# Kernel tuning notes

Hardware: AMD Instinct MI355X
Metric: run time of the kernel (lower is better)

Reference implementation:

```python
import jax, jax.numpy as jnp
import numpy as np

N = 50000      # nodes
E = 400000     # edges per relation
R = 3          # edge types
D = 128        # input_dim == hidden_dim
H = 8          # attention heads
Dh = D // H    # per-head dim (16)
OUT = 1        # output logits
NEG_SLOPE = 0.2
LN_EPS = 1e-5


def setup_inputs() -> dict:
    key = jax.random.key(0)
    ks = jax.random.split(key, 20)
    s = 0.05
    f32 = jnp.float32
    return {
        "feat": jax.random.normal(ks[0], (N, D), f32),
        "edge_src": jax.random.randint(ks[1], (R, E), 0, N, dtype=jnp.int32),
        "edge_dst": jax.random.randint(ks[2], (R, E), 0, N, dtype=jnp.int32),
        # conv1: per-relation GATConv params (W, attn_l, attn_r, bias)
        "W1": jax.random.normal(ks[3], (R, D, H * Dh), f32) * s,
        "al1": jax.random.normal(ks[4], (R, H, Dh), f32) * s,
        "ar1": jax.random.normal(ks[5], (R, H, Dh), f32) * s,
        "b1": jnp.zeros((R, H * Dh), f32),
        # conv2
        "W2": jax.random.normal(ks[6], (R, D, H * Dh), f32) * s,
        "al2": jax.random.normal(ks[7], (R, H, Dh), f32) * s,
        "ar2": jax.random.normal(ks[8], (R, H, Dh), f32) * s,
        "b2": jnp.zeros((R, H * Dh), f32),
        # LayerNorm
        "ln_g": jnp.ones((D,), f32),
        "ln_b": jnp.zeros((D,), f32),
        # classifier MLP (dropout inactive at eval)
        "Wc1": jax.random.normal(ks[9], (D, D), f32) * s,
        "bc1": jnp.zeros((D,), f32),
        "Wc2": jax.random.normal(ks[10], (D, OUT), f32) * s,
        "bc2": jnp.zeros((OUT,), f32),
    }


def _gat(x, src, dst, W, al, ar, b):
    """DGL GATConv on one relation: x [N,Din] -> [N, H*Dh]."""
    h = (x @ W).reshape(N, H, Dh)                       # projected feats
    el = (h * al).sum(-1)                               # [N,H] src attn term
    er = (h * ar).sum(-1)                               # [N,H] dst attn term
    e = jax.nn.leaky_relu(el[src] + er[dst], NEG_SLOPE)  # [E,H]
    # edge-softmax over incoming edges per dst node, per head
    m = jax.ops.segment_max(e, dst, num_segments=N)     # [N,H]
    ex = jnp.exp(e - m[dst])
    denom = jax.ops.segment_sum(ex, dst, num_segments=N)
    alpha = ex / denom[dst]                             # [E,H]
    msg = alpha[:, :, None] * h[src]                    # [E,H,Dh]
    out = jax.ops.segment_sum(msg, dst, num_segments=N)  # [N,H,Dh]
    return out.reshape(N, H * Dh) + b


def _hetero(x, edge_src, edge_dst, W, al, ar, b):
    out = jnp.zeros((N, H * Dh), x.dtype)
    for r in range(R):  # small fixed relation count
        out = out + _gat(x, edge_src[r], edge_dst[r], W[r], al[r], ar[r], b[r])
    return out


def reference(feat, edge_src, edge_dst, W1, al1, ar1, b1, W2, al2, ar2, b2,
              ln_g, ln_b, Wc1, bc1, Wc2, bc2):
    h1 = jax.nn.relu(_hetero(feat, edge_src, edge_dst, W1, al1, ar1, b1))
    h2 = _hetero(h1, edge_src, edge_dst, W2, al2, ar2, b2)
    h = h2 + h1
    mu = h.mean(-1, keepdims=True)
    var = ((h - mu) ** 2).mean(-1, keepdims=True)
    h = (h - mu) * jax.lax.rsqrt(var + LN_EPS) * ln_g + ln_b
    h = jax.nn.relu(h @ Wc1 + bc1)
    return h @ Wc2 + bc2
```

## Files before the change

kernel.cpp:

```cpp
#include <hip/hip_runtime.h>
#include <math.h>

#define NN 50000
#define NE 400000
#define NREL 3
#define NCH 196

typedef __bf16 bf16x8 __attribute__((ext_vector_type(8)));
typedef float floatx4 __attribute__((ext_vector_type(4)));

__device__ __forceinline__ unsigned short f2bf(float f) {
  unsigned int u = __float_as_uint(f);
  return (unsigned short)((u + 0x7fffu + ((u >> 16) & 1u)) >> 16);
}

__global__ __launch_bounds__(256) void prep_wt(
    const float* __restrict__ W1, const float* __restrict__ W2,
    const float* __restrict__ Wc1, unsigned short* __restrict__ Wt,
    int* __restrict__ cnt) {
  int mat = blockIdx.x >> 3, slab = blockIdx.x & 7;
  const float* Wsrc = mat < 3 ? W1 + mat * 16384
                    : (mat < 6 ? W2 + (mat - 3) * 16384 : Wc1);
  unsigned short* dst = Wt + (size_t)mat * 144 * 128;
  int k0 = slab * 16;
#pragma unroll
  for (int i = 0; i < 8; ++i) {
    int idx = i * 256 + threadIdx.x;
    int k = k0 + (idx >> 7), nn = idx & 127;
    dst[nn * 128 + k] = f2bf(Wsrc[k * 128 + nn]);
  }
  for (int i = blockIdx.x * 256 + threadIdx.x; i < NREL * NN; i += 56 * 256)
    cnt[i] = 0;
}

__global__ __launch_bounds__(256) void prep_attn(
    const float* __restrict__ W1, const float* __restrict__ W2,
    const float* __restrict__ al1, const float* __restrict__ ar1,
    const float* __restrict__ al2, const float* __restrict__ ar2,
    unsigned short* __restrict__ Wt) {
  int blk = blockIdx.x;
  int mat = blk >> 3;
  int half = (blk >> 2) & 1;
  int kslab = blk & 3;
  const float* Wsrc = mat < 3 ? W1 + mat * 16384 : W2 + (mat - 3) * 16384;
  const float* av = half ? (mat < 3 ? ar1 + mat * 128 : ar2 + (mat - 3) * 128)
                         : (mat < 3 ? al1 + mat * 128 : al2 + (mat - 3) * 128);
  int h = threadIdx.x & 7;
  int k = kslab * 32 + (threadIdx.x >> 3);
  float s = 0.f;
#pragma unroll
  for (int j = 0; j < 4; ++j) {
    float4 w = *(const float4*)&Wsrc[k * 128 + h * 16 + j * 4];
    float4 a = *(const float4*)&av[h * 16 + j * 4];
    s += w.x * a.x + w.y * a.y + w.z * a.z + w.w * a.w;
  }
  Wt[(size_t)mat * 144 * 128 + (128 + half * 8 + h) * 128 + k] = f2bf(s);
}

__global__ __launch_bounds__(256, 4) void gemm3_attn_mfma(
    const float* __restrict__ X, const unsigned short* __restrict__ Wt,
    unsigned short* __restrict__ hp, float* __restrict__ el,
    float* __restrict__ er, int n) {
  __shared__ unsigned short Ws[144 * 136];
  int t = threadIdx.x;
  int lane = t & 63, wave = t >> 6;
  int quad = lane >> 4, l = lane & 15;
  int rowbase = blockIdx.x * 64;
  int myrow = rowbase + wave * 16 + l;

  bf16x8 afr[4];
  const float4* X4 = (const float4*)X;
#pragma unroll
  for (int ks = 0; ks < 4; ++ks) {
    float4 x0 = make_float4(0.f, 0.f, 0.f, 0.f), x1 = x0;
    if (myrow < n) {
      size_t base = (size_t)myrow * 32 + ks * 8 + quad * 2;
      x0 = X4[base];
      x1 = X4[base + 1];
    }
    union { unsigned short u[8]; bf16x8 v; } cv;
    cv.u[0] = f2bf(x0.x); cv.u[1] = f2bf(x0.y);
    cv.u[2] = f2bf(x0.z); cv.u[3] = f2bf(x0.w);
    cv.u[4] = f2bf(x1.x); cv.u[5] = f2bf(x1.y);
    cv.u[6] = f2bf(x1.z); cv.u[7] = f2bf(x1.w);
    afr[ks] = cv.v;
  }

  for (int r = 0; r < NREL; ++r) {
    if (r > 0) __syncthreads();
    const uint4* WtR = (const uint4*)(Wt + (size_t)r * 144 * 128);
#pragma unroll
    for (int i = 0; i < 9; ++i) {
      int v = t + i * 256;
      ((uint4*)Ws)[(v >> 4) * 17 + (v & 15)] = WtR[v];
    }
    __syncthreads();

    floatx4 acc[9];
#pragma unroll
    for (int i = 0; i < 9; ++i) acc[i] = floatx4{0.f, 0.f, 0.f, 0.f};
#pragma unroll
    for (int ks = 0; ks < 4; ++ks) {
#pragma unroll
      for (int nt = 0; nt < 9; ++nt) {
        bf16x8 b = *(const bf16x8*)&Ws[(nt * 16 + l) * 136 + ks * 32 + quad * 8];
        acc[nt] = __builtin_amdgcn_mfma_f32_16x16x32_bf16(afr[ks], b, acc[nt], 0, 0, 0);
      }
    }

    unsigned short* hpR = hp + (size_t)r * NN * 128;
    float* elR = el + (size_t)r * NN * 8;
    float* erR = er + (size_t)r * NN * 8;
    int r0 = rowbase + wave * 16 + quad * 4;
#pragma unroll
    for (int reg = 0; reg < 4; ++reg) {
      int row = r0 + reg;
      if (row < n) {
#pragma unroll
        for (int nt = 0; nt < 8; ++nt)
          hpR[(size_t)row * 128 + nt * 16 + l] = f2bf(acc[nt][reg]);
        if (l < 8) elR[row * 8 + l] = acc[8][reg];
        else       erR[row * 8 + (l - 8)] = acc[8][reg];
      }
    }
  }
}

__global__ __launch_bounds__(256) void gemm_head_mfma(
    const float* __restrict__ X, const unsigned short* __restrict__ Wt,
    const float* __restrict__ bc1, const float* __restrict__ wc2,
    const float* __restrict__ bc2, float* __restrict__ out, int n) {
  __shared__ unsigned short Xs[64 * 136];
  __shared__ unsigned short Ws[128 * 136];
  int t = threadIdx.x;
  int rowbase = blockIdx.x * 64;

  const float4* X4 = (const float4*)X;
#pragma unroll
  for (int i = 0; i < 8; ++i) {
    int v = t + i * 256;
    int row = v >> 5, k4 = (v & 31) * 4;
    float4 x = make_float4(0.f, 0.f, 0.f, 0.f);
    if (rowbase + row < n) x = X4[(size_t)(rowbase + row) * 32 + (v & 31)];
    ushort4 p;
    p.x = f2bf(x.x); p.y = f2bf(x.y); p.z = f2bf(x.z); p.w = f2bf(x.w);
    *(ushort4*)&Xs[row * 136 + k4] = p;
  }
  const uint4* WtR = (const uint4*)Wt;
#pragma unroll
  for (int i = 0; i < 8; ++i) {
    int v = t + i * 256;
    ((uint4*)Ws)[(v >> 4) * 17 + (v & 15)] = WtR[v];
  }
  __syncthreads();

  int lane = t & 63, wave = t >> 6;
  int quad = lane >> 4, l = lane & 15;

  floatx4 acc[8];
#pragma unroll
  for (int i = 0; i < 8; ++i) acc[i] = floatx4{0.f, 0.f, 0.f, 0.f};
#pragma unroll
  for (int ks = 0; ks < 4; ++ks) {
    bf16x8 a = *(const bf16x8*)&Xs[(wave * 16 + l) * 136 + ks * 32 + quad * 8];
#pragma unroll
    for (int nt = 0; nt < 8; ++nt) {
      bf16x8 b = *(const bf16x8*)&Ws[(nt * 16 + l) * 136 + ks * 32 + quad * 8];
      acc[nt] = __builtin_amdgcn_mfma_f32_16x16x32_bf16(a, b, acc[nt], 0, 0, 0);
    }
  }

  float bv[8], wv[8];
#pragma unroll
  for (int nt = 0; nt < 8; ++nt) {
    bv[nt] = bc1[nt * 16 + l];
    wv[nt] = wc2[nt * 16 + l];
  }
  int r0 = rowbase + wave * 16 + quad * 4;
#pragma unroll
  for (int reg = 0; reg < 4; ++reg) {
    float s = 0.f;
#pragma unroll
    for (int nt = 0; nt < 8; ++nt)
      s += fmaxf(acc[nt][reg] + bv[nt], 0.f) * wv[nt];
    s += __shfl_xor(s, 1); s += __shfl_xor(s, 2);
    s += __shfl_xor(s, 4); s += __shfl_xor(s, 8);
    int row = r0 + reg;
    if (l == 0 && row < n) out[row] = s + bc2[0];
  }
}

__global__ __launch_bounds__(256) void hist_kernel(
    const int* __restrict__ edst, int* __restrict__ cnt, int* __restrict__ rank) {
  int t = blockIdx.x * 256 + threadIdx.x;
  if (t >= NREL * NE) return;
  int r = t / NE;
  rank[t] = atomicAdd(&cnt[r * NN + edst[t]], 1);
}

__global__ __launch_bounds__(256) void scan1(
    const int* __restrict__ cnt, int* __restrict__ partials) {
  __shared__ int s[256];
  int r = blockIdx.x / NCH, c = blockIdx.x % NCH;
  int i = c * 256 + threadIdx.x;
  s[threadIdx.x] = (i < NN) ? cnt[r * NN + i] : 0;
  __syncthreads();
  for (int off = 128; off; off >>= 1) {
    if (threadIdx.x < off) s[threadIdx.x] += s[threadIdx.x + off];
    __syncthreads();
  }
  if (threadIdx.x == 0) partials[r * NCH + c] = s[0];
}

__global__ __launch_bounds__(256) void scan2(int* __restrict__ partials) {
  __shared__ int s[256];
  int r = blockIdx.x;
  int t = threadIdx.x;
  int v = (t < NCH) ? partials[r * NCH + t] : 0;
  s[t] = v;
  __syncthreads();
  for (int off = 1; off < 256; off <<= 1) {
    int x = (t >= off) ? s[t - off] : 0;
    __syncthreads();
    s[t] += x;
    __syncthreads();
  }
  if (t < NCH) partials[r * NCH + t] = s[t] - v;
}

__global__ __launch_bounds__(256) void scan3(
    const int* __restrict__ cnt, const int* __restrict__ partials,
    int* __restrict__ rowptr) {
  __shared__ int s[256];
  int r = blockIdx.x / NCH, c = blockIdx.x % NCH;
  int t = threadIdx.x;
  int i = c * 256 + t;
  int v = (i < NN) ? cnt[r * NN + i] : 0;
  s[t] = v;
  __syncthreads();
  for (int off = 1; off < 256; off <<= 1) {
    int x = (t >= off) ? s[t - off] : 0;
    __syncthreads();
    s[t] += x;
    __syncthreads();
  }
  int base = partials[r * NCH + c];
  if (i < NN) rowptr[r * (NN + 1) + i] = base + s[t] - v;
  if (c == NCH - 1 && t == 0) rowptr[r * (NN + 1) + NN] = NE;
}

__global__ __launch_bounds__(256) void scatter_kernel(
    const int* __restrict__ esrc, const int* __restrict__ edst,
    const int* __restrict__ rowptr, const int* __restrict__ rank,
    int* __restrict__ col) {
  int t = blockIdx.x * 256 + threadIdx.x;
  if (t >= NREL * NE) return;
  int r = t / NE;
  int pos = rowptr[r * (NN + 1) + edst[t]] + rank[t];
  col[(size_t)r * NE + pos] = esrc[t];
}

__global__ __launch_bounds__(256) void gather_all(
    const int* __restrict__ rowptr, const int* __restrict__ col,
    const float* __restrict__ el, const float* __restrict__ er,
    const unsigned short* __restrict__ hp, const float* __restrict__ b,
    float* __restrict__ h1, const float* __restrict__ g,
    const float* __restrict__ beta, int mode) {
  int wid = (blockIdx.x * 256 + threadIdx.x) >> 6;
  int lane = threadIdx.x & 63;
  if (wid >= NN) return;
  int h = lane >> 3;
  int eoff = lane & 7;
  int c = lane * 2;

  int st3[NREL], en3[NREL], cv3[NREL];
  float er3[NREL];
#pragma unroll
  for (int r = 0; r < NREL; ++r) {
    const int* rp = rowptr + r * (NN + 1);
    st3[r] = rp[wid];
    en3[r] = rp[wid + 1];
    er3[r] = er[(size_t)r * NN * 8 + wid * 8 + h];
  }
#pragma unroll
  for (int r = 0; r < NREL; ++r) {
    int last = en3[r] - 1;
    last = last < st3[r] ? st3[r] : last;
    int i0 = st3[r] + eoff;
    cv3[r] = col[r * NE + (i0 < last ? i0 : last)];
  }

  float ax = 0.f, ay = 0.f;
#pragma unroll
  for (int r = 0; r < NREL; ++r) {
    int start = st3[r], end = en3[r];
    if (end > start) {
      const int* cl = col + r * NE;
      const float* elr = el + (size_t)r * NN * 8;
      const unsigned short* hpr = hp + (size_t)r * NN * 128;
      float er_me = er3[r];
      int last = end - 1;
      int idx = start + eoff;
      int colv = cv3[r];
      float den = 0.f, sx = 0.f, sy = 0.f;
      for (int i = start; i < end; i += 8) {
        int nidx = idx + 8;
        int colm = cl[nidx < last ? nidx : last];
        float e = elr[colv * 8 + h] + er_me;
        e = fmaxf(e, 0.2f * e);
        float x = (idx < end) ? __expf(e) : 0.f;
        den += x;
        unsigned int xi = __float_as_uint(x);
#define GATHER_EDGE(JJ)                                                        \
        {                                                                      \
          int sj = __builtin_amdgcn_readlane(colv, JJ);                        \
          const unsigned int* rowp = (const unsigned int*)(hpr + (size_t)sj * 128); \
          unsigned int u = rowp[lane];                                         \
          float xe = __uint_as_float(                                          \
              __builtin_amdgcn_ds_swizzle(xi, ((JJ) << 5) | 0x18));            \
          sx += xe * __uint_as_float(u << 16);                                 \
          sy += xe * __uint_as_float(u & 0xffff0000u);                         \
        }
        GATHER_EDGE(0)
        GATHER_EDGE(1)
        GATHER_EDGE(2)
        GATHER_EDGE(3)
        GATHER_EDGE(4)
        GATHER_EDGE(5)
        GATHER_EDGE(6)
        GATHER_EDGE(7)
#undef GATHER_EDGE
        idx = nidx;
        colv = colm;
      }
      den += __shfl_xor(den, 1);
      den += __shfl_xor(den, 2);
      den += __shfl_xor(den, 4);
      float inv = 1.f / den;
      ax += sx * inv;
      ay += sy * inv;
    }
  }

  float bx = b[c] + b[128 + c] + b[256 + c];
  float by = b[c + 1] + b[128 + c + 1] + b[256 + c + 1];
  float2* hptr = (float2*)&h1[(size_t)wid * 128 + c];
  if (mode == 0) {
    *hptr = make_float2(fmaxf(ax + bx, 0.f), fmaxf(ay + by, 0.f));
  } else {
    float2 r1 = *hptr;
    float vx = ax + bx + r1.x;
    float vy = ay + by + r1.y;
    float s = vx + vy;
#pragma unroll
    for (int off = 32; off; off >>= 1) s += __shfl_xor(s, off);
    float mu = s * (1.f / 128.f);
    float dx = vx - mu, dy = vy - mu;
    float sq = dx * dx + dy * dy;
#pragma unroll
    for (int off = 32; off; off >>= 1) sq += __shfl_xor(sq, off);
    float rstd = rsqrtf(sq * (1.f / 128.f) + 1e-5f);
    *hptr = make_float2(dx * rstd * g[c] + beta[c],
                        dy * rstd * g[c + 1] + beta[c + 1]);
  }
}

extern "C" void kernel_launch(void* const* d_in, const int* in_sizes, int n_in,
                              void* d_out, int out_size, void* d_ws, size_t ws_size,
                              hipStream_t stream) {
  const float* feat = (const float*)d_in[0];
  const int* esrc = (const int*)d_in[1];
  const int* edst = (const int*)d_in[2];
  const float* W1 = (const float*)d_in[3];
  const float* al1 = (const float*)d_in[4];
  const float* ar1 = (const float*)d_in[5];
  const float* b1 = (const float*)d_in[6];
  const float* W2 = (const float*)d_in[7];
  const float* al2 = (const float*)d_in[8];
  const float* ar2 = (const float*)d_in[9];
  const float* b2 = (const float*)d_in[10];
  const float* lng = (const float*)d_in[11];
  const float* lnb = (const float*)d_in[12];
  const float* Wc1 = (const float*)d_in[13];
  const float* bc1 = (const float*)d_in[14];
  const float* Wc2 = (const float*)d_in[15];
  const float* bc2 = (const float*)d_in[16];
  float* out = (float*)d_out;

  unsigned short* hp = (unsigned short*)d_ws;
  float* el = (float*)(hp + (size_t)3 * NN * 128);
  float* er = el + (size_t)3 * NN * 8;
  float* h1 = er + (size_t)3 * NN * 8;
  int* rowptr = (int*)(h1 + (size_t)NN * 128);
  int* col = rowptr + NREL * (NN + 1);
  int* cnt = col + (size_t)NREL * NE;
  int* partials = cnt + NREL * NN;
  unsigned short* Wt = (unsigned short*)(((uintptr_t)(partials + NREL * NCH) + 15)
                                         & ~(uintptr_t)15);
  int* rank = (int*)el;

  const int gemm3_grid = (NN + 63) / 64;
  const int head_grid = (NN + 63) / 64;
  const int edge_grid = (NREL * NE + 255) / 256;
  const int gg_grid = (NN * 64) / 256;

  prep_wt<<<56, 256, 0, stream>>>(W1, W2, Wc1, Wt, cnt);
  prep_attn<<<48, 256, 0, stream>>>(W1, W2, al1, ar1, al2, ar2, Wt);

  hist_kernel<<<edge_grid, 256, 0, stream>>>(edst, cnt, rank);
  scan1<<<NREL * NCH, 256, 0, stream>>>(cnt, partials);
  scan2<<<NREL, 256, 0, stream>>>(partials);
  scan3<<<NREL * NCH, 256, 0, stream>>>(cnt, partials, rowptr);
  scatter_kernel<<<edge_grid, 256, 0, stream>>>(esrc, edst, rowptr, rank, col);

  gemm3_attn_mfma<<<gemm3_grid, 256, 0, stream>>>(feat, Wt, hp, el, er, NN);
  gather_all<<<gg_grid, 256, 0, stream>>>(rowptr, col, el, er, hp, b1,
                                          h1, nullptr, nullptr, 0);
  gemm3_attn_mfma<<<gemm3_grid, 256, 0, stream>>>(
      h1, Wt + (size_t)3 * 144 * 128, hp, el, er, NN);
  gather_all<<<gg_grid, 256, 0, stream>>>(rowptr, col, el, er, hp, b2,
                                          h1, lng, lnb, 1);
  gemm_head_mfma<<<head_grid, 256, 0, stream>>>(
      h1, Wt + (size_t)6 * 144 * 128, bc1, Wc2, bc2, out, NN);
}
```

Before: 364.1 us.

## Build CSR with atomic-cursor scatter, vectorized edge reads, merged scan passes

The histogram kernel no longer stores per-edge ranks; it reads four destinations at a time with int4 loads and only increments counts. The first two scan stages are merged into one kernel per relation in which each thread serially sums a 256-element chunk. The final scan writes exclusive offsets into the count array, which the scatter kernel then uses as atomic cursors to place source ids. This removes the rank array traffic and one launch, at the cost of a second round of atomics and a CSR column order within each row that is no longer deterministic, which can slightly change floating-point summation order in the gather.

```diff
diff --git a/kernel.cpp b/kernel.cpp
--- a/kernel.cpp
+++ b/kernel.cpp
@@ -191,33 +191,30 @@
 }
 
 __global__ __launch_bounds__(256) void hist_kernel(
-    const int* __restrict__ edst, int* __restrict__ cnt, int* __restrict__ rank) {
+    const int* __restrict__ edst, int* __restrict__ cnt) {
   int t = blockIdx.x * 256 + threadIdx.x;
-  if (t >= NREL * NE) return;
-  int r = t / NE;
-  rank[t] = atomicAdd(&cnt[r * NN + edst[t]], 1);
-}
-
-__global__ __launch_bounds__(256) void scan1(
+  if (t >= NREL * NE / 4) return;
+  int r = t / (NE / 4);
+  int e4 = t - r * (NE / 4);
+  int4 d = ((const int4*)(edst + (size_t)r * NE))[e4];
+  int* cr = cnt + r * NN;
+  atomicAdd(&cr[d.x], 1);
+  atomicAdd(&cr[d.y], 1);
+  atomicAdd(&cr[d.z], 1);
+  atomicAdd(&cr[d.w], 1);
+}
+
+__global__ __launch_bounds__(256) void scanA(
     const int* __restrict__ cnt, int* __restrict__ partials) {
   __shared__ int s[256];
-  int r = blockIdx.x / NCH, c = blockIdx.x % NCH;
-  int i = c * 256 + threadIdx.x;
-  s[threadIdx.x] = (i < NN) ? cnt[r * NN + i] : 0;
-  __syncthreads();
-  for (int off = 128; off; off >>= 1) {
-    if (threadIdx.x < off) s[threadIdx.x] += s[threadIdx.x + off];
-    __syncthreads();
-  }
-  if (threadIdx.x == 0) partials[r * NCH + c] = s[0];
-}
-
-__global__ __launch_bounds__(256) void scan2(int* __restrict__ partials) {
-  __shared__ int s[256];
-  int r = blockIdx.x;
-  int t = threadIdx.x;
-  int v = (t < NCH) ? partials[r * NCH + t] : 0;
-  s[t] = v;
+  int r = blockIdx.x, t = threadIdx.x;
+  int sum = 0;
+  if (t < NCH) {
+    const int* base = cnt + r * NN + t * 256;
+    int lim = NN - t * 256; lim = lim < 256 ? lim : 256;
+    for (int j = 0; j < lim; ++j) sum += base[j];
+  }
+  s[t] = sum;
   __syncthreads();
   for (int off = 1; off < 256; off <<= 1) {
     int x = (t >= off) ? s[t - off] : 0;
@@ -225,11 +222,11 @@
     s[t] += x;
     __syncthreads();
   }
-  if (t < NCH) partials[r * NCH + t] = s[t] - v;
+  if (t < NCH) partials[r * NCH + t] = s[t] - sum;
 }
 
 __global__ __launch_bounds__(256) void scan3(
-    const int* __restrict__ cnt, const int* __restrict__ partials,
+    int* __restrict__ cnt, const int* __restrict__ partials,
     int* __restrict__ rowptr) {
   __shared__ int s[256];
   int r = blockIdx.x / NCH, c = blockIdx.x % NCH;
@@ -245,19 +242,29 @@
     __syncthreads();
   }
   int base = partials[r * NCH + c];
-  if (i < NN) rowptr[r * (NN + 1) + i] = base + s[t] - v;
+  if (i < NN) {
+    int val = base + s[t] - v;
+    rowptr[r * (NN + 1) + i] = val;
+    cnt[r * NN + i] = val;
+  }
   if (c == NCH - 1 && t == 0) rowptr[r * (NN + 1) + NN] = NE;
 }
 
 __global__ __launch_bounds__(256) void scatter_kernel(
     const int* __restrict__ esrc, const int* __restrict__ edst,
-    const int* __restrict__ rowptr, const int* __restrict__ rank,
-    int* __restrict__ col) {
+    int* __restrict__ rp2, int* __restrict__ col) {
   int t = blockIdx.x * 256 + threadIdx.x;
-  if (t >= NREL * NE) return;
-  int r = t / NE;
-  int pos = rowptr[r * (NN + 1) + edst[t]] + rank[t];
-  col[(size_t)r * NE + pos] = esrc[t];
+  if (t >= NREL * NE / 4) return;
+  int r = t / (NE / 4);
+  int e4 = t - r * (NE / 4);
+  int4 s4 = ((const int4*)(esrc + (size_t)r * NE))[e4];
+  int4 d4 = ((const int4*)(edst + (size_t)r * NE))[e4];
+  int* rr = rp2 + r * NN;
+  int* colr = col + (size_t)r * NE;
+  colr[atomicAdd(&rr[d4.x], 1)] = s4.x;
+  colr[atomicAdd(&rr[d4.y], 1)] = s4.y;
+  colr[atomicAdd(&rr[d4.z], 1)] = s4.z;
+  colr[atomicAdd(&rr[d4.w], 1)] = s4.w;
 }
 
 __global__ __launch_bounds__(256) void gather_all(
@@ -397,21 +404,19 @@
   int* partials = cnt + NREL * NN;
   unsigned short* Wt = (unsigned short*)(((uintptr_t)(partials + NREL * NCH) + 15)
                                          & ~(uintptr_t)15);
-  int* rank = (int*)el;
 
   const int gemm3_grid = (NN + 63) / 64;
   const int head_grid = (NN + 63) / 64;
-  const int edge_grid = (NREL * NE + 255) / 256;
+  const int edge4_grid = (NREL * NE / 4 + 255) / 256;
   const int gg_grid = (NN * 64) / 256;
 
   prep_wt<<<56, 256, 0, stream>>>(W1, W2, Wc1, Wt, cnt);
   prep_attn<<<48, 256, 0, stream>>>(W1, W2, al1, ar1, al2, ar2, Wt);
 
-  hist_kernel<<<edge_grid, 256, 0, stream>>>(edst, cnt, rank);
-  scan1<<<NREL * NCH, 256, 0, stream>>>(cnt, partials);
-  scan2<<<NREL, 256, 0, stream>>>(partials);
+  hist_kernel<<<edge4_grid, 256, 0, stream>>>(edst, cnt);
+  scanA<<<NREL, 256, 0, stream>>>(cnt, partials);
   scan3<<<NREL * NCH, 256, 0, stream>>>(cnt, partials, rowptr);
-  scatter_kernel<<<edge_grid, 256, 0, stream>>>(esrc, edst, rowptr, rank, col);
+  scatter_kernel<<<edge4_grid, 256, 0, stream>>>(esrc, edst, cnt, col);
 
   gemm3_attn_mfma<<<gemm3_grid, 256, 0, stream>>>(feat, Wt, hp, el, er, NN);
   gather_all<<<gg_grid, 256, 0, stream>>>(rowptr, col, el, er, hp, b1,
```

After: 440.1 us. +20.9%, slower.
